# Optimization experiments

Hardware: AMD Instinct MI355X
Metric: run time of the kernel (lower is better)

## Reference

```python
import jax, jax.numpy as jnp
import numpy as np

N = 50000
E = 800000
D = 64


def setup_inputs() -> dict:
    key = jax.random.key(0)
    ks = jax.random.split(key, 8)
    x = jax.random.normal(ks[0], (N, D), dtype=jnp.float32)
    edge_index = jax.random.randint(ks[1], (2, E), 0, N, dtype=jnp.int32)
    s = 1.0 / np.sqrt(D)
    Wl1 = jax.random.normal(ks[2], (D, D), dtype=jnp.float32) * s
    Wr1 = jax.random.normal(ks[3], (D, D), dtype=jnp.float32) * s
    b1 = jnp.zeros((D,), dtype=jnp.float32)
    Wl2 = jax.random.normal(ks[4], (D, D), dtype=jnp.float32) * s
    Wr2 = jax.random.normal(ks[5], (D, D), dtype=jnp.float32) * s
    b2 = jnp.zeros((D,), dtype=jnp.float32)
    return {"x": x, "edge_index": edge_index, "Wl1": Wl1, "Wr1": Wr1,
            "b1": b1, "Wl2": Wl2, "Wr2": Wr2, "b2": b2}


def sage_conv(x, src, dst, inv_deg, Wl, Wr, b):
    # mean aggregation of source features onto destination nodes
    msgs = x[src]                                   # [E, D] gather
    agg = jax.ops.segment_sum(msgs, dst, num_segments=N)  # [N, D]
    agg = agg * inv_deg[:, None]                    # mean
    return agg @ Wl + x @ Wr + b


def reference(x, edge_index, Wl1, Wr1, b1, Wl2, Wr2, b2):
    src, dst = edge_index[0], edge_index[1]
    deg = jax.ops.segment_sum(jnp.ones((E,), jnp.float32), dst, num_segments=N)
    inv_deg = jnp.where(deg > 0, 1.0 / jnp.maximum(deg, 1.0), 0.0)
    h = jax.nn.relu(sage_conv(x, src, dst, inv_deg, Wl1, Wr1, b1))
    out = sage_conv(h, src, dst, inv_deg, Wl2, Wr2, b2)
    return out
```

## Files before the change

### kernel.cpp

```cpp
#include <hip/hip_runtime.h>
#include <hip/hip_bf16.h>

#define NN 50000
#define EE 800000
#define DD 64
#define NB32 1563
#define PA_BLOCKS 256
#define PA_CHUNK (EE / PA_BLOCKS)
#define CAP32 768
#define CVT_XBLOCKS 3125
#define FRONT_BLOCKS (CVT_XBLOCKS + 8 + 1)

typedef short bf16x8 __attribute__((ext_vector_type(8)));
typedef float f32x4 __attribute__((ext_vector_type(4)));

__device__ inline unsigned short f2bf(float f) {
    unsigned u = __float_as_uint(f);
    return (unsigned short)((u + 0x7FFF + ((u >> 16) & 1)) >> 16);
}
__device__ inline float bflo(unsigned u) { return __uint_as_float(u << 16); }
__device__ inline float bfhi(unsigned u) { return __uint_as_float(u & 0xFFFF0000u); }
__device__ inline unsigned bfpack(float a, float b) {
    return (unsigned)f2bf(a) | ((unsigned)f2bf(b) << 16);
}

__global__ void front_kernel(const float* __restrict__ x,
                             const float* __restrict__ Wl1,
                             const float* __restrict__ Wr1,
                             const float* __restrict__ Wl2,
                             const float* __restrict__ Wr2,
                             unsigned short* __restrict__ xbf,
                             unsigned short* __restrict__ wbf_t,
                             int* __restrict__ binCursor) {
    const int tid = threadIdx.x;
    const int bid = blockIdx.x;
    if (bid < CVT_XBLOCKS) {
        int i = bid * 256 + tid;
        if (i < NN * DD / 4) {
            float4 v = reinterpret_cast<const float4*>(x)[i];
            ushort4 u;
            u.x = f2bf(v.x); u.y = f2bf(v.y); u.z = f2bf(v.z); u.w = f2bf(v.w);
            reinterpret_cast<ushort4*>(xbf)[i] = u;
        }
    } else if (bid < CVT_XBLOCKS + 8) {
        int j = (bid - CVT_XBLOCKS) * 256 + tid;
        int m   = j >> 10;
        int col = (j >> 4) & 63;
        int kg  = j & 15;
        const float* WlX = m ? Wl2 : Wl1;
        const float* WrX = m ? Wr2 : Wr1;
        unsigned short t8[8];
        #pragma unroll
        for (int t = 0; t < 8; ++t) {
            int k = kg * 8 + t;
            float v = (k < 64) ? WlX[k * 64 + col] : WrX[(k - 64) * 64 + col];
            t8[t] = f2bf(v);
        }
        uint4 u;
        u.x = (unsigned)t8[0] | ((unsigned)t8[1] << 16);
        u.y = (unsigned)t8[2] | ((unsigned)t8[3] << 16);
        u.z = (unsigned)t8[4] | ((unsigned)t8[5] << 16);
        u.w = (unsigned)t8[6] | ((unsigned)t8[7] << 16);
        reinterpret_cast<uint4*>(wbf_t)[j] = u;
    } else {
        for (int i = tid; i < NB32; i += 256) binCursor[i] = i * CAP32;
    }
}

__global__ void binscatter_kernel(const int* __restrict__ src, const int* __restrict__ dst,
                                  int* __restrict__ binCursor, unsigned* __restrict__ ebuf) {
    __shared__ int hist[NB32];
    __shared__ int base[NB32];
    const int tid = threadIdx.x;
    for (int i = tid; i < NB32; i += 256) hist[i] = 0;
    __syncthreads();
    const int e0 = blockIdx.x * PA_CHUNK;
    for (int e = e0 + tid; e < e0 + PA_CHUNK; e += 256)
        atomicAdd(&hist[dst[e] >> 5], 1);
    __syncthreads();
    for (int i = tid; i < NB32; i += 256) {
        int c = hist[i];
        base[i] = c ? atomicAdd(&binCursor[i], c) : 0;
        hist[i] = 0;
    }
    __syncthreads();
    for (int e = e0 + tid; e < e0 + PA_CHUNK; e += 256) {
        int d = dst[e];
        int b = d >> 5;
        int off = atomicAdd(&hist[b], 1);
        ebuf[base[b] + off] = ((unsigned)(d & 31) << 16) | (unsigned)src[e];
    }
}

__launch_bounds__(256, 5)
__global__ void fused_layer_kernel(const unsigned* __restrict__ ebuf,
                                   const int* __restrict__ binCursor,
                                   unsigned short* __restrict__ esrc,
                                   int* __restrict__ offs,
                                   const unsigned short* __restrict__ feat,
                                   const unsigned short* __restrict__ selfb,
                                   const unsigned short* __restrict__ Wbf,
                                   const float* __restrict__ bias,
                                   float* __restrict__ outp,
                                   unsigned short* __restrict__ outbf,
                                   int relu, int sortMode) {
    __shared__ unsigned short eidx[CAP32];
    __shared__ int h32[32];
    __shared__ int loff[33];
    __shared__ unsigned short Albs[32 * 128];
    __shared__ unsigned short Wlds[64 * 128];
    const int tid = threadIdx.x;
    const int g = blockIdx.x;
    const int nbase = g * 32;
    const int e0 = g * CAP32;
    const int cnt = binCursor[g] - e0;
    char* Ab = reinterpret_cast<char*>(Albs);
    char* Wb = reinterpret_cast<char*>(Wlds);

    if (sortMode) {
        unsigned* scratch = reinterpret_cast<unsigned*>(Wlds);
        for (int i = tid; i < cnt; i += 256) scratch[i] = ebuf[e0 + i];
        if (tid < 32) h32[tid] = 0;
        __syncthreads();
        for (int i = tid; i < cnt; i += 256)
            atomicAdd(&h32[(scratch[i] >> 16) & 31], 1);
        __syncthreads();
        if (tid == 0) {
            int run = 0;
            #pragma unroll
            for (int i = 0; i < 32; ++i) { loff[i] = run; run += h32[i]; }
            loff[32] = run;
        }
        __syncthreads();
        if (tid < 32) {
            offs[nbase + tid] = e0 + loff[tid];
            h32[tid] = loff[tid];
        }
        __syncthreads();
        for (int i = tid; i < cnt; i += 256) {
            unsigned p = scratch[i];
            int n = (p >> 16) & 31;
            int pos = atomicAdd(&h32[n], 1);
            eidx[pos] = (unsigned short)(p & 0xFFFFu);
        }
        __syncthreads();
        for (int i = tid; i < cnt; i += 256) esrc[e0 + i] = eidx[i];
    } else {
        if (tid < 32) loff[tid] = offs[nbase + tid] - e0;
        if (tid == 0) loff[32] = cnt;
        __syncthreads();
        for (int i = tid; i < cnt; i += 256) eidx[i] = esrc[e0 + i];
        __syncthreads();
    }

    #pragma unroll
    for (int i = 0; i < 4; ++i) {
        int idx = i * 256 + tid;
        uint4 u = reinterpret_cast<const uint4*>(Wbf)[idx];
        int col = idx >> 4, kg = idx & 15;
        int byte = (col * 256 + kg * 16) ^ ((col & 7) << 4);
        *reinterpret_cast<uint4*>(Wb + byte) = u;
    }
    {
        int n  = tid >> 3;
        int kq = tid & 7;
        int node = nbase + n;
        uint4 u = make_uint4(0u, 0u, 0u, 0u);
        if (node < NN)
            u = *reinterpret_cast<const uint4*>(selfb + (size_t)node * DD + kq * 8);
        int byte = (n * 256 + (8 + kq) * 16) ^ ((n & 7) << 4);
        *reinterpret_cast<uint4*>(Ab + byte) = u;
    }

    {
        const int nl = tid >> 3;
        const int q  = tid & 7;
        const int qo = q << 3;
        const int le0 = loff[nl], le1 = loff[nl + 1];
        float a0 = 0.f, a1 = 0.f, a2 = 0.f, a3 = 0.f;
        float a4 = 0.f, a5 = 0.f, a6 = 0.f, a7 = 0.f;
        int e = le0;
        for (; e + 7 < le1; e += 8) {
            uint4 u0 = *reinterpret_cast<const uint4*>(feat + (size_t)eidx[e + 0] * DD + qo);
            uint4 u1 = *reinterpret_cast<const uint4*>(feat + (size_t)eidx[e + 1] * DD + qo);
            uint4 u2 = *reinterpret_cast<const uint4*>(feat + (size_t)eidx[e + 2] * DD + qo);
            uint4 u3 = *reinterpret_cast<const uint4*>(feat + (size_t)eidx[e + 3] * DD + qo);
            uint4 u4 = *reinterpret_cast<const uint4*>(feat + (size_t)eidx[e + 4] * DD + qo);
            uint4 u5 = *reinterpret_cast<const uint4*>(feat + (size_t)eidx[e + 5] * DD + qo);
            uint4 u6 = *reinterpret_cast<const uint4*>(feat + (size_t)eidx[e + 6] * DD + qo);
            uint4 u7 = *reinterpret_cast<const uint4*>(feat + (size_t)eidx[e + 7] * DD + qo);
            a0 += ((bflo(u0.x) + bflo(u1.x)) + (bflo(u2.x) + bflo(u3.x)))
                + ((bflo(u4.x) + bflo(u5.x)) + (bflo(u6.x) + bflo(u7.x)));
            a1 += ((bfhi(u0.x) + bfhi(u1.x)) + (bfhi(u2.x) + bfhi(u3.x)))
                + ((bfhi(u4.x) + bfhi(u5.x)) + (bfhi(u6.x) + bfhi(u7.x)));
            a2 += ((bflo(u0.y) + bflo(u1.y)) + (bflo(u2.y) + bflo(u3.y)))
                + ((bflo(u4.y) + bflo(u5.y)) + (bflo(u6.y) + bflo(u7.y)));
            a3 += ((bfhi(u0.y) + bfhi(u1.y)) + (bfhi(u2.y) + bfhi(u3.y)))
                + ((bfhi(u4.y) + bfhi(u5.y)) + (bfhi(u6.y) + bfhi(u7.y)));
            a4 += ((bflo(u0.z) + bflo(u1.z)) + (bflo(u2.z) + bflo(u3.z)))
                + ((bflo(u4.z) + bflo(u5.z)) + (bflo(u6.z) + bflo(u7.z)));
            a5 += ((bfhi(u0.z) + bfhi(u1.z)) + (bfhi(u2.z) + bfhi(u3.z)))
                + ((bfhi(u4.z) + bfhi(u5.z)) + (bfhi(u6.z) + bfhi(u7.z)));
            a6 += ((bflo(u0.w) + bflo(u1.w)) + (bflo(u2.w) + bflo(u3.w)))
                + ((bflo(u4.w) + bflo(u5.w)) + (bflo(u6.w) + bflo(u7.w)));
            a7 += ((bfhi(u0.w) + bfhi(u1.w)) + (bfhi(u2.w) + bfhi(u3.w)))
                + ((bfhi(u4.w) + bfhi(u5.w)) + (bfhi(u6.w) + bfhi(u7.w)));
        }
        for (; e + 1 < le1; e += 2) {
            uint4 u0 = *reinterpret_cast<const uint4*>(feat + (size_t)eidx[e + 0] * DD + qo);
            uint4 u1 = *reinterpret_cast<const uint4*>(feat + (size_t)eidx[e + 1] * DD + qo);
            a0 += bflo(u0.x) + bflo(u1.x); a1 += bfhi(u0.x) + bfhi(u1.x);
            a2 += bflo(u0.y) + bflo(u1.y); a3 += bfhi(u0.y) + bfhi(u1.y);
            a4 += bflo(u0.z) + bflo(u1.z); a5 += bfhi(u0.z) + bfhi(u1.z);
            a6 += bflo(u0.w) + bflo(u1.w); a7 += bfhi(u0.w) + bfhi(u1.w);
        }
        if (e < le1) {
            uint4 u0 = *reinterpret_cast<const uint4*>(feat + (size_t)eidx[e] * DD + qo);
            a0 += bflo(u0.x); a1 += bfhi(u0.x);
            a2 += bflo(u0.y); a3 += bfhi(u0.y);
            a4 += bflo(u0.z); a5 += bfhi(u0.z);
            a6 += bflo(u0.w); a7 += bfhi(u0.w);
        }
        float iv = (le1 > le0) ? (1.0f / (float)(le1 - le0)) : 0.0f;
        uint4 pk;
        pk.x = bfpack(a0 * iv, a1 * iv);
        pk.y = bfpack(a2 * iv, a3 * iv);
        pk.z = bfpack(a4 * iv, a5 * iv);
        pk.w = bfpack(a6 * iv, a7 * iv);
        int byte = (nl * 256 + q * 16) ^ ((nl & 7) << 4);
        *reinterpret_cast<uint4*>(Ab + byte) = pk;
    }
    __syncthreads();

    {
        const int lane = tid & 63;
        const int w = tid >> 6;
        const int mt = w & 1;
        const int nt0 = (w >> 1) * 2;
        const int lr = lane & 15;
        const int lg = lane >> 4;

        const int arow = mt * 16 + lr;
        const int c0 = nt0 * 16 + lr;
        const int c1 = c0 + 16;
        f32x4 acc0, acc1;
        {
            float b0 = bias[c0], b1 = bias[c1];
            #pragma unroll
            for (int r = 0; r < 4; ++r) { acc0[r] = b0; acc1[r] = b1; }
        }
        const int aswz = (arow & 7) << 4;
        const int b0swz = (c0 & 7) << 4;
        const int b1swz = (c1 & 7) << 4;
        #pragma unroll
        for (int ks = 0; ks < 4; ++ks) {
            int kg = ks * 4 + lg;
            bf16x8 a = *reinterpret_cast<const bf16x8*>(
                Ab + ((arow * 256 + kg * 16) ^ aswz));
            bf16x8 b0 = *reinterpret_cast<const bf16x8*>(
                Wb + ((c0 * 256 + kg * 16) ^ b0swz));
            bf16x8 b1 = *reinterpret_cast<const bf16x8*>(
                Wb + ((c1 * 256 + kg * 16) ^ b1swz));
            acc0 = __builtin_amdgcn_mfma_f32_16x16x32_bf16(a, b0, acc0, 0, 0, 0);
            acc1 = __builtin_amdgcn_mfma_f32_16x16x32_bf16(a, b1, acc1, 0, 0, 0);
        }
        #pragma unroll
        for (int r = 0; r < 4; ++r) {
            int node = nbase + mt * 16 + lg * 4 + r;
            if (node < NN) {
                float v0 = acc0[r], v1 = acc1[r];
                if (relu) { v0 = fmaxf(v0, 0.f); v1 = fmaxf(v1, 0.f); }
                if (outp) {
                    outp[(size_t)node * DD + c0] = v0;
                    outp[(size_t)node * DD + c1] = v1;
                }
                if (outbf) {
                    outbf[(size_t)node * DD + c0] = f2bf(v0);
                    outbf[(size_t)node * DD + c1] = f2bf(v1);
                }
            }
        }
    }
}

static inline size_t rup(size_t b) { return (b + 255) & ~(size_t)255; }

extern "C" void kernel_launch(void* const* d_in, const int* in_sizes, int n_in,
                              void* d_out, int out_size, void* d_ws, size_t ws_size,
                              hipStream_t stream) {
    const float* x   = (const float*)d_in[0];
    const int*   ei  = (const int*)d_in[1];
    const float* Wl1 = (const float*)d_in[2];
    const float* Wr1 = (const float*)d_in[3];
    const float* b1  = (const float*)d_in[4];
    const float* Wl2 = (const float*)d_in[5];
    const float* Wr2 = (const float*)d_in[6];
    const float* b2  = (const float*)d_in[7];
    float* out = (float*)d_out;

    const int* src = ei;
    const int* dst = ei + EE;

    char* p = (char*)d_ws;
    int* binCursor        = (int*)p;            p += rup((size_t)NB32 * 4);
    unsigned* ebuf        = (unsigned*)p;       p += rup((size_t)NB32 * CAP32 * 4);
    unsigned short* esrc  = (unsigned short*)p; p += rup((size_t)NB32 * CAP32 * 2);
    int* offs             = (int*)p;            p += rup((size_t)NB32 * 32 * 4);
    unsigned short* xbf   = (unsigned short*)p; p += rup((size_t)NN * DD * 2);
    unsigned short* hbf   = (unsigned short*)p; p += rup((size_t)NN * DD * 2);
    unsigned short* wbf_t = (unsigned short*)p; p += rup((size_t)2 * 64 * 128 * 2);

    front_kernel<<<FRONT_BLOCKS, 256, 0, stream>>>(x, Wl1, Wr1, Wl2, Wr2,
                                                   xbf, wbf_t, binCursor);
    binscatter_kernel<<<PA_BLOCKS, 256, 0, stream>>>(src, dst, binCursor, ebuf);

    fused_layer_kernel<<<NB32, 256, 0, stream>>>(ebuf, binCursor, esrc, offs,
                                                 xbf, xbf, wbf_t, b1,
                                                 nullptr, hbf, 1, 1);
    fused_layer_kernel<<<NB32, 256, 0, stream>>>(ebuf, binCursor, esrc, offs,
                                                 hbf, hbf, wbf_t + 8192, b2,
                                                 out, nullptr, 0, 0);
}
```

Before: 68.54 us.

## Sort nodes by degree within each block and stage dst indices in LDS

Inside the fused layer kernel, each block now ranks its 32 nodes by in-degree and maps thread groups to nodes in that order. Nodes of similar degree then share a wavefront, which reduces divergence in the gather loop. The binscatter kernel also copies its chunk of dst indices into shared memory once instead of reading them from global memory twice. Costs are an extra O(32) rank computation per block, more LDS use, and an extra indirection when reading the node id.

```diff
diff --git a/kernel.cpp b/kernel.cpp
--- a/kernel.cpp
+++ b/kernel.cpp
@@ -71,12 +71,14 @@
                                   int* __restrict__ binCursor, unsigned* __restrict__ ebuf) {
     __shared__ int hist[NB32];
     __shared__ int base[NB32];
+    __shared__ int dloc[PA_CHUNK];
     const int tid = threadIdx.x;
+    const int e0 = blockIdx.x * PA_CHUNK;
     for (int i = tid; i < NB32; i += 256) hist[i] = 0;
+    for (int i = tid; i < PA_CHUNK; i += 256) dloc[i] = dst[e0 + i];
     __syncthreads();
-    const int e0 = blockIdx.x * PA_CHUNK;
-    for (int e = e0 + tid; e < e0 + PA_CHUNK; e += 256)
-        atomicAdd(&hist[dst[e] >> 5], 1);
+    for (int i = tid; i < PA_CHUNK; i += 256)
+        atomicAdd(&hist[dloc[i] >> 5], 1);
     __syncthreads();
     for (int i = tid; i < NB32; i += 256) {
         int c = hist[i];
@@ -84,11 +86,11 @@
         hist[i] = 0;
     }
     __syncthreads();
-    for (int e = e0 + tid; e < e0 + PA_CHUNK; e += 256) {
-        int d = dst[e];
+    for (int i = tid; i < PA_CHUNK; i += 256) {
+        int d = dloc[i];
         int b = d >> 5;
         int off = atomicAdd(&hist[b], 1);
-        ebuf[base[b] + off] = ((unsigned)(d & 31) << 16) | (unsigned)src[e];
+        ebuf[base[b] + off] = ((unsigned)(d & 31) << 16) | (unsigned)src[e0 + i];
     }
 }
 
@@ -107,6 +109,7 @@
     __shared__ unsigned short eidx[CAP32];
     __shared__ int h32[32];
     __shared__ int loff[33];
+    __shared__ unsigned char perm[32];
     __shared__ unsigned short Albs[32 * 128];
     __shared__ unsigned short Wlds[64 * 128];
     const int tid = threadIdx.x;
@@ -136,6 +139,17 @@
             offs[nbase + tid] = e0 + loff[tid];
             h32[tid] = loff[tid];
         }
+        if (tid >= 64 && tid < 96) {
+            int i = tid - 64;
+            int deg = loff[i + 1] - loff[i];
+            int r = 0;
+            #pragma unroll 8
+            for (int j = 0; j < 32; ++j) {
+                int dj = loff[j + 1] - loff[j];
+                r += (dj > deg) || (dj == deg && j < i);
+            }
+            perm[r] = (unsigned char)i;
+        }
         __syncthreads();
         for (int i = tid; i < cnt; i += 256) {
             unsigned p = scratch[i];
@@ -150,6 +164,17 @@
         if (tid == 0) loff[32] = cnt;
         __syncthreads();
         for (int i = tid; i < cnt; i += 256) eidx[i] = esrc[e0 + i];
+        if (tid >= 64 && tid < 96) {
+            int i = tid - 64;
+            int deg = loff[i + 1] - loff[i];
+            int r = 0;
+            #pragma unroll 8
+            for (int j = 0; j < 32; ++j) {
+                int dj = loff[j + 1] - loff[j];
+                r += (dj > deg) || (dj == deg && j < i);
+            }
+            perm[r] = (unsigned char)i;
+        }
         __syncthreads();
     }
 
@@ -173,7 +198,7 @@
     }
 
     {
-        const int nl = tid >> 3;
+        const int nl = perm[tid >> 3];
         const int q  = tid & 7;
         const int qo = q << 3;
         const int le0 = loff[nl], le1 = loff[nl + 1];
```

Measured after the change: 70.33 us (median of 2 runs). +2.6%, slower.
